# Kernel optimization log

Measured on AMD Instinct MI355X. Metric: run time of the kernel, lower is better.

Reference implementation:

```python
import jax, jax.numpy as jnp
import numpy as np

DIM = 1024
NUM_HEADS = 16
HEAD_DIM = DIM // NUM_HEADS


def _rope(x):
    # x: (B*H, L, hd). ESM-style rotary embedding with rotate_half.
    L, hd = x.shape[1], x.shape[2]
    inv_freq = 1.0 / (10000.0 ** (jnp.arange(0, hd, 2, dtype=jnp.float32) / hd))
    t = jnp.arange(L, dtype=jnp.float32)
    freqs = t[:, None] * inv_freq[None, :]          # (L, hd/2)
    emb = jnp.concatenate([freqs, freqs], axis=-1)   # (L, hd)
    cos, sin = jnp.cos(emb), jnp.sin(emb)
    x1, x2 = jnp.split(x, 2, axis=-1)
    rot = jnp.concatenate([-x2, x1], axis=-1)
    return x * cos + rot * sin


def setup_inputs() -> dict:
    key = jax.random.key(0)
    ks = jax.random.split(key, 10)
    L, N, D = 2048, 1, DIM
    query = jax.random.normal(ks[0], (L, N, D), dtype=jnp.float32)
    asym_ids = jnp.sort(jax.random.randint(ks[1], (N, L), 0, 4), axis=-1)
    s = 0.02
    wq = s * jax.random.normal(ks[2], (D, D), dtype=jnp.float32)
    wk = s * jax.random.normal(ks[3], (D, D), dtype=jnp.float32)
    wv = s * jax.random.normal(ks[4], (D, D), dtype=jnp.float32)
    wo = s * jax.random.normal(ks[5], (D, D), dtype=jnp.float32)
    bq = s * jax.random.normal(ks[6], (D,), dtype=jnp.float32)
    bk = s * jax.random.normal(ks[7], (D,), dtype=jnp.float32)
    bv = s * jax.random.normal(ks[8], (D,), dtype=jnp.float32)
    bo = s * jax.random.normal(ks[9], (D,), dtype=jnp.float32)
    return {"query": query, "asym_ids": asym_ids, "wq": wq, "bq": bq,
            "wk": wk, "bk": bk, "wv": wv, "bv": bv, "wo": wo, "bo": bo}


def reference(query, asym_ids, wq, bq, wk, bk, wv, bv, wo, bo):
    L, N, D = query.shape
    H, hd = NUM_HEADS, HEAD_DIM
    scaling = 1.0 / np.sqrt(hd)

    q = (query @ wq.T + bq) * scaling
    k = query @ wk.T + bk
    v = query @ wv.T + bv

    def to_bh(x):  # (L, N, D) -> (N*H, L, hd)
        return x.reshape(L, N * H, hd).transpose(1, 0, 2)

    q, k, v = to_bh(q), to_bh(k), to_bh(v)

    # raw scores (pre-RoPE), rpe scores (post-RoPE)
    raw = jnp.einsum('ble,bme->blm', q, k).reshape(N, H, L, L)
    qr, kr = _rope(q), _rope(k)
    rpe = jnp.einsum('ble,bme->blm', qr, kr).reshape(N, H, L, L)

    avg = jnp.mean(rpe - raw, axis=(0, 1), keepdims=True)          # (1,1,L,L)
    asym_mask = asym_ids[:, :, None] == asym_ids[:, None, :]        # (N,L,L)
    attn_weights = jnp.where(asym_mask[:, None], rpe, raw + avg)    # (N,H,L,L)

    probs = jax.nn.softmax(attn_weights, axis=-1)
    attn = jnp.einsum('nhlm,nhme->nhle', probs, v.reshape(N, H, L, hd))
    attn = attn.transpose(2, 0, 1, 3).reshape(L, N, D)
    out = attn @ wo.T + bo
    attn_weights_avg = jnp.mean(probs, axis=1)  # (N, L, L)
    return out, attn_weights_avg
```

## Files before the change

### kernel.cpp

```cpp
#include <hip/hip_runtime.h>
#include <hip/hip_bf16.h>

#define L 2048
#define D 1024
#define NH 16
#define HD 64
#define SPLIT 4
#define JCH (L / SPLIT)
#define LOG2E 1.4426950408889634f

typedef __attribute__((ext_vector_type(8))) short bf16x8;
typedef __attribute__((ext_vector_type(4))) float f32x4;

#define MFMA(a, b, c) __builtin_amdgcn_mfma_f32_16x16x32_bf16(a, b, c, 0, 0, 0)

__device__ __forceinline__ short f2bf(float x) {
  __hip_bfloat16 h = __float2bfloat16(x);
  return *reinterpret_cast<short*>(&h);
}

__device__ __forceinline__ void gll16(const void* g, void* l) {
  __builtin_amdgcn_global_load_lds(
      (const __attribute__((address_space(1))) void*)(uintptr_t)g,
      (__attribute__((address_space(3))) void*)(unsigned)(uintptr_t)l, 16, 0, 0);
}

__global__ void prep_kernel(const float* __restrict__ q,
                            const float* __restrict__ w0, const float* __restrict__ w1,
                            const float* __restrict__ w2, const float* __restrict__ w3,
                            float* __restrict__ costab, float* __restrict__ sintab,
                            short* __restrict__ dq, short* __restrict__ d0,
                            short* __restrict__ d1, short* __restrict__ d2,
                            short* __restrict__ d3) {
  int i = blockIdx.x * 256 + threadIdx.x;
  if (i < 65536) {
    int t = i >> 5, fi = i & 31;
    float f = exp2f(-(float)fi * (13.287712379549449f / 32.0f));
    float ang = (float)t * f;
    costab[i] = cosf(ang);
    sintab[i] = sinf(ang);
    return;
  }
  int i2 = i - 65536;
  const float* src;
  short* dst;
  int off;
  if (i2 < L * D / 4) {
    src = q; dst = dq; off = i2;
  } else {
    int j = i2 - L * D / 4;
    int seg = j >> 18;
    off = j & (262144 - 1);
    src = seg == 0 ? w0 : seg == 1 ? w1 : seg == 2 ? w2 : w3;
    dst = seg == 0 ? d0 : seg == 1 ? d1 : seg == 2 ? d2 : d3;
  }
  float4 v = ((const float4*)src)[off];
  short4 o;
  o.x = f2bf(v.x); o.y = f2bf(v.y); o.z = f2bf(v.z); o.w = f2bf(v.w);
  ((short4*)dst)[off] = o;
}

__global__ __launch_bounds__(256) void proj3_kernel(
    const short* __restrict__ X,
    const short* __restrict__ Wq, const short* __restrict__ Wk, const short* __restrict__ Wv,
    const float* __restrict__ bq, const float* __restrict__ bk, const float* __restrict__ bv,
    const float* __restrict__ costab, const float* __restrict__ sintab,
    short* __restrict__ Qs, short* __restrict__ QRb, short* __restrict__ Kbb,
    short* __restrict__ KRb, short* __restrict__ Vt) {
  int mode = blockIdx.z;
  const short* W = mode == 0 ? Wq : (mode == 1 ? Wk : Wv);
  const float* bias = mode == 0 ? bq : (mode == 1 ? bk : bv);
  short* out_main = mode == 0 ? Qs : (mode == 1 ? Kbb : Vt);
  short* out_rope = mode == 0 ? QRb : KRb;

  int w = threadIdx.x >> 6, lane = threadIdx.x & 63;
  int c = lane & 15, g = lane >> 4;
  int wi0 = blockIdx.y * 128 + w * 32;
  int wj0 = blockIdx.x * 64;

  f32x4 acc[2][4];
#pragma unroll
  for (int m = 0; m < 2; ++m)
#pragma unroll
    for (int n = 0; n < 4; ++n) acc[m][n] = (f32x4){0.f, 0.f, 0.f, 0.f};

  for (int k0 = 0; k0 < D; k0 += 32) {
    bf16x8 aF[2], bF[4];
#pragma unroll
    for (int m = 0; m < 2; ++m)
      aF[m] = *(const bf16x8*)(X + (size_t)(wi0 + m * 16 + c) * D + k0 + g * 8);
#pragma unroll
    for (int n = 0; n < 4; ++n)
      bF[n] = *(const bf16x8*)(W + (size_t)(wj0 + n * 16 + c) * D + k0 + g * 8);
#pragma unroll
    for (int m = 0; m < 2; ++m)
#pragma unroll
      for (int n = 0; n < 4; ++n) acc[m][n] = MFMA(aF[m], bF[n], acc[m][n]);
  }

  float scale = (mode == 0) ? 0.125f * LOG2E : 1.0f;
#pragma unroll
  for (int m = 0; m < 2; ++m) {
#pragma unroll
    for (int r = 0; r < 4; ++r) {
      int i = wi0 + m * 16 + g * 4 + r;
      float v4[4];
#pragma unroll
      for (int n = 0; n < 4; ++n)
        v4[n] = (acc[m][n][r] + bias[wj0 + n * 16 + c]) * scale;
      if (mode == 2) {
#pragma unroll
        for (int n = 0; n < 4; ++n) {
          int col = wj0 + n * 16 + c;
          out_main[(size_t)col * L + i] = f2bf(v4[n]);
        }
      } else {
#pragma unroll
        for (int n = 0; n < 4; ++n) {
          int col = wj0 + n * 16 + c;
          out_main[(size_t)i * D + col] = f2bf(v4[n]);
          float rot = (n < 2) ? -v4[n + 2] : v4[n - 2];
          int fidx = i * 32 + (n & 1) * 16 + c;
          float vr = v4[n] * costab[fidx] + rot * sintab[fidx];
          out_rope[(size_t)i * D + col] = f2bf(vr);
        }
      }
    }
  }
}

__global__ __launch_bounds__(256) void avg_kernel(
    const short* __restrict__ QR, const short* __restrict__ KR,
    const short* __restrict__ Qs, const short* __restrict__ Kb,
    const int* __restrict__ ids, f32x4* __restrict__ avg4) {
  int ib = blockIdx.y * 128, jb = blockIdx.x * 64;
  if (ids[ib] == ids[ib + 127] && ids[jb] == ids[jb + 63] && ids[ib] == ids[jb])
    return;

  int w = threadIdx.x >> 6, lane = threadIdx.x & 63;
  int c = lane & 15, g = lane >> 4;
  int wi0 = ib + (w >> 1) * 64;
  int wj0 = jb + (w & 1) * 32;

  f32x4 acc1[4][2], acc2[4][2];
#pragma unroll
  for (int m = 0; m < 4; ++m)
#pragma unroll
    for (int n = 0; n < 2; ++n) {
      acc1[m][n] = (f32x4){0.f, 0.f, 0.f, 0.f};
      acc2[m][n] = (f32x4){0.f, 0.f, 0.f, 0.f};
    }

  for (int k0 = 0; k0 < D; k0 += 32) {
    bf16x8 aF[4], a2F[4], bF[2], b2F[2];
#pragma unroll
    for (int m = 0; m < 4; ++m) {
      aF[m] = *(const bf16x8*)(QR + (size_t)(wi0 + m * 16 + c) * D + k0 + g * 8);
      a2F[m] = *(const bf16x8*)(Qs + (size_t)(wi0 + m * 16 + c) * D + k0 + g * 8);
    }
#pragma unroll
    for (int n = 0; n < 2; ++n) {
      bF[n] = *(const bf16x8*)(KR + (size_t)(wj0 + n * 16 + c) * D + k0 + g * 8);
      b2F[n] = *(const bf16x8*)(Kb + (size_t)(wj0 + n * 16 + c) * D + k0 + g * 8);
    }
#pragma unroll
    for (int m = 0; m < 4; ++m)
#pragma unroll
      for (int n = 0; n < 2; ++n) {
        acc1[m][n] = MFMA(aF[m], bF[n], acc1[m][n]);
        acc2[m][n] = MFMA(a2F[m], b2F[n], acc2[m][n]);
      }
  }

#pragma unroll
  for (int m = 0; m < 4; ++m)
#pragma unroll
    for (int n = 0; n < 2; ++n) {
      int j = wj0 + n * 16 + c;
      f32x4 o;
#pragma unroll
      for (int r = 0; r < 4; ++r) o[r] = (acc1[m][n][r] - acc2[m][n][r]) * 0.0625f;
      avg4[(size_t)(((wi0 + m * 16) >> 2) + g) * L + j] = o;
    }
}

__global__ __launch_bounds__(256) void flash3_kernel(
    const short* __restrict__ Qs, const short* __restrict__ Kb,
    const short* __restrict__ QR, const short* __restrict__ KR,
    const short* __restrict__ Vt, const f32x4* __restrict__ avg4,
    const int* __restrict__ ids, float* __restrict__ m_part,
    float* __restrict__ l_part, float* __restrict__ acc_part) {
  int dd = blockIdx.x + 32 * (blockIdx.y + NH * blockIdx.z);
  int xcd = dd & 7, slot = dd >> 3;
  int xblk = xcd * 4 + (slot & 3);
  int hs = slot >> 2;
  int h = hs & (NH - 1), sp = hs >> 4;

  int w = threadIdx.x >> 6, lane = threadIdx.x & 63;
  int c = lane & 15, g = lane >> 4;
  int i0 = xblk * 64 + w * 16;
  int hk = h * 64;

  __shared__ short kb_lds[2][64 * 64];
  __shared__ short kr_lds[2][64 * 64];
  __shared__ short plds[4][16][64];

  int srow = lane >> 3;
  int sxor = (lane & 7) ^ srow;
  int r0a = w * 16, r0b = w * 16 + 8;

  bf16x8 qA[2], qrA[2];
  {
    const short* qp = Qs + (size_t)(i0 + c) * D + hk + g * 8;
    const short* qrp = QR + (size_t)(i0 + c) * D + hk + g * 8;
    qA[0] = *(const bf16x8*)qp;   qA[1] = *(const bf16x8*)(qp + 32);
    qrA[0] = *(const bf16x8*)qrp; qrA[1] = *(const bf16x8*)(qrp + 32);
  }

  int idi[4];
  float mrun[4], lsum[4];
  f32x4 acc[4];
#pragma unroll
  for (int r = 0; r < 4; ++r) {
    idi[r] = ids[i0 + g * 4 + r];
    mrun[r] = -3.0e38f;
    lsum[r] = 0.f;
  }
#pragma unroll
  for (int n = 0; n < 4; ++n) acc[n] = (f32x4){0.f, 0.f, 0.f, 0.f};

  int ifirst = __shfl(idi[0], 0);
  bool iu = __all((idi[0] == idi[1]) & (idi[1] == idi[2]) & (idi[2] == idi[3]) &
                  (idi[0] == ifirst));

  const f32x4* avrow = avg4 + (size_t)((i0 >> 2) + g) * L;
  int jbase = sp * JCH;
  const int NT = JCH / 64;

  gll16(Kb + (size_t)(jbase + r0a + srow) * D + hk + sxor * 8, &kb_lds[0][r0a * 64]);
  gll16(Kb + (size_t)(jbase + r0b + srow) * D + hk + sxor * 8, &kb_lds[0][r0b * 64]);
  gll16(KR + (size_t)(jbase + r0a + srow) * D + hk + sxor * 8, &kr_lds[0][r0a * 64]);
  gll16(KR + (size_t)(jbase + r0b + srow) * D + hk + sxor * 8, &kr_lds[0][r0b * 64]);

  f32x4 avn[4];
  int idjn[4];
#pragma unroll
  for (int sub = 0; sub < 4; ++sub) {
    avn[sub] = avrow[jbase + sub * 16 + c];
    idjn[sub] = ids[jbase + sub * 16 + c];
  }
  __syncthreads();

  int cur = 0;
  for (int jt = 0; jt < NT; ++jt) {
    int jb = jbase + jt * 64;

    if (jt + 1 < NT) {
      int jn = jb + 64;
      short* kd = &kb_lds[cur ^ 1][0];
      short* rd = &kr_lds[cur ^ 1][0];
      gll16(Kb + (size_t)(jn + r0a + srow) * D + hk + sxor * 8, kd + r0a * 64);
      gll16(Kb + (size_t)(jn + r0b + srow) * D + hk + sxor * 8, kd + r0b * 64);
      gll16(KR + (size_t)(jn + r0a + srow) * D + hk + sxor * 8, rd + r0a * 64);
      gll16(KR + (size_t)(jn + r0b + srow) * D + hk + sxor * 8, rd + r0b * 64);
    }

    bf16x8 vf0[4], vf1[4];
#pragma unroll
    for (int n = 0; n < 4; ++n) {
      const short* vp = Vt + (size_t)(hk + n * 16 + c) * L + jb + g * 8;
      vf0[n] = *(const bf16x8*)vp;
      vf1[n] = *(const bf16x8*)(vp + 32);
    }

    f32x4 av[4];
    int idj[4];
#pragma unroll
    for (int sub = 0; sub < 4; ++sub) { av[sub] = avn[sub]; idj[sub] = idjn[sub]; }
    if (jt + 1 < NT) {
#pragma unroll
      for (int sub = 0; sub < 4; ++sub) {
        avn[sub] = avrow[jb + 64 + sub * 16 + c];
        idjn[sub] = ids[jb + 64 + sub * 16 + c];
      }
    }

    int jfirst = __shfl(idj[0], 0);
    bool ju = __all((idj[0] == idj[1]) & (idj[1] == idj[2]) & (idj[2] == idj[3]) &
                    (idj[0] == jfirst));

    const short* kbb = &kb_lds[cur][c * 64];
    const short* krb = &kr_lds[cur][c * 64];
    int co0 = (g ^ (c & 7)) * 8;
    int co1 = ((4 + g) ^ (c & 7)) * 8;

    float t[4][4];
    if (iu && ju && ifirst == jfirst) {
#pragma unroll
      for (int sub = 0; sub < 4; ++sub) {
        bf16x8 kr0 = *(const bf16x8*)(krb + sub * 1024 + co0);
        bf16x8 kr1 = *(const bf16x8*)(krb + sub * 1024 + co1);
        f32x4 z = (f32x4){0.f, 0.f, 0.f, 0.f};
        f32x4 rp = MFMA(qrA[1], kr1, MFMA(qrA[0], kr0, z));
#pragma unroll
        for (int r = 0; r < 4; ++r) t[sub][r] = rp[r];
      }
    } else if (iu && ju) {
#pragma unroll
      for (int sub = 0; sub < 4; ++sub) {
        bf16x8 k0 = *(const bf16x8*)(kbb + sub * 1024 + co0);
        bf16x8 k1 = *(const bf16x8*)(kbb + sub * 1024 + co1);
        f32x4 z = (f32x4){0.f, 0.f, 0.f, 0.f};
        f32x4 rw = MFMA(qA[1], k1, MFMA(qA[0], k0, z));
#pragma unroll
        for (int r = 0; r < 4; ++r) t[sub][r] = rw[r] + av[sub][r];
      }
    } else {
#pragma unroll
      for (int sub = 0; sub < 4; ++sub) {
        bf16x8 k0 = *(const bf16x8*)(kbb + sub * 1024 + co0);
        bf16x8 k1 = *(const bf16x8*)(kbb + sub * 1024 + co1);
        bf16x8 kr0 = *(const bf16x8*)(krb + sub * 1024 + co0);
        bf16x8 kr1 = *(const bf16x8*)(krb + sub * 1024 + co1);
        f32x4 z = (f32x4){0.f, 0.f, 0.f, 0.f};
        f32x4 rw = MFMA(qA[1], k1, MFMA(qA[0], k0, z));
        f32x4 rp = MFMA(qrA[1], kr1, MFMA(qrA[0], kr0, z));
#pragma unroll
        for (int r = 0; r < 4; ++r)
          t[sub][r] = (idi[r] == idj[sub]) ? rp[r] : (rw[r] + av[sub][r]);
      }
    }

    float tm[4];
#pragma unroll
    for (int r = 0; r < 4; ++r)
      tm[r] = fmaxf(fmaxf(t[0][r], t[1][r]), fmaxf(t[2][r], t[3][r]));
    bool ok = (tm[0] <= mrun[0] + 8.f) && (tm[1] <= mrun[1] + 8.f) &&
              (tm[2] <= mrun[2] + 8.f) && (tm[3] <= mrun[3] + 8.f);
    if (!__all(ok)) {
#pragma unroll
      for (int r = 0; r < 4; ++r) {
        float m2 = tm[r];
#pragma unroll
        for (int d = 1; d < 16; d <<= 1) m2 = fmaxf(m2, __shfl_xor(m2, d));
        float mn = fmaxf(mrun[r], m2);
        float so = exp2f(mrun[r] - mn);
        mrun[r] = mn;
        lsum[r] *= so;
#pragma unroll
        for (int n = 0; n < 4; ++n) acc[n][r] *= so;
      }
    }

#pragma unroll
    for (int sub = 0; sub < 4; ++sub)
#pragma unroll
      for (int r = 0; r < 4; ++r) {
        float p = exp2f(t[sub][r] - mrun[r]);
        lsum[r] += p;
        int prow = g * 4 + r;
        plds[w][prow][(sub * 16 + c) ^ ((prow & 7) << 3)] = f2bf(p);
      }

    {
      int pc0 = (g * 8) ^ ((c & 7) << 3);
      int pc1 = (32 + g * 8) ^ ((c & 7) << 3);
      bf16x8 pa = *(const bf16x8*)(&plds[w][c][pc0]);
#pragma unroll
      for (int n = 0; n < 4; ++n) acc[n] = MFMA(pa, vf0[n], acc[n]);
      bf16x8 pb = *(const bf16x8*)(&plds[w][c][pc1]);
#pragma unroll
      for (int n = 0; n < 4; ++n) acc[n] = MFMA(pb, vf1[n], acc[n]);
    }

    __syncthreads();
    cur ^= 1;
  }

#pragma unroll
  for (int r = 0; r < 4; ++r) {
#pragma unroll
    for (int d = 1; d < 16; d <<= 1) lsum[r] += __shfl_xor(lsum[r], d);
  }
  size_t sb = (size_t)(sp * NH + h) * L;
  if (c == 0) {
#pragma unroll
    for (int r = 0; r < 4; ++r) {
      m_part[sb + i0 + g * 4 + r] = mrun[r];
      l_part[sb + i0 + g * 4 + r] = lsum[r];
    }
  }
#pragma unroll
  for (int n = 0; n < 4; ++n)
#pragma unroll
    for (int r = 0; r < 4; ++r)
      acc_part[(sb + i0 + g * 4 + r) * HD + n * 16 + c] = acc[n][r];
}

__global__ void merge_kernel(const float* __restrict__ m_part,
                             const float* __restrict__ l_part,
                             const float* __restrict__ acc_part,
                             float* __restrict__ mfin, float* __restrict__ lfin,
                             short* __restrict__ attn_bf) {
  int idx = blockIdx.x * 256 + threadIdx.x;
  int d = idx & (HD - 1);
  int hi = idx >> 6;
  int i = hi & (L - 1), h = hi >> 11;
  float m4 = -3.0e38f;
#pragma unroll
  for (int s = 0; s < SPLIT; ++s)
    m4 = fmaxf(m4, m_part[(size_t)(s * NH + h) * L + i]);
  float l = 0.f, o = 0.f;
#pragma unroll
  for (int s = 0; s < SPLIT; ++s) {
    size_t sb = (size_t)(s * NH + h) * L + i;
    float e = exp2f(m_part[sb] - m4);
    l += l_part[sb] * e;
    o += acc_part[sb * HD + d] * e;
  }
  attn_bf[(size_t)i * D + h * HD + d] = f2bf(o / l);
  if (d == 0) { mfin[h * L + i] = m4; lfin[h * L + i] = l; }
}

__global__ __launch_bounds__(256) void pavgout_kernel(
    const short* __restrict__ Qs, const short* __restrict__ Kb,
    const short* __restrict__ QR, const short* __restrict__ KR,
    const f32x4* __restrict__ avg4, const int* __restrict__ ids,
    const float* __restrict__ m_ws, const float* __restrict__ l_ws,
    float* __restrict__ out1,
    const short* __restrict__ A, const short* __restrict__ W,
    const float* __restrict__ bias, float* __restrict__ out0) {
  __shared__ short kb_lds[2][64 * 64];
  __shared__ short kr_lds[2][64 * 64];
  __shared__ float mS[NH][64], lS[NH][64];

  int bid = blockIdx.x;
  int w = threadIdx.x >> 6, lane = threadIdx.x & 63;
  int c = lane & 15, g = lane >> 4;

  if (bid >= 1024) {
    int idx = bid - 1024;
    int wj0 = (idx & 15) * 64 + (w & 1) * 32;
    int wi0 = (idx >> 4) * 64 + (w >> 1) * 32;

    f32x4 acc[2][2];
#pragma unroll
    for (int m = 0; m < 2; ++m)
#pragma unroll
      for (int n = 0; n < 2; ++n) acc[m][n] = (f32x4){0.f, 0.f, 0.f, 0.f};

    for (int k0 = 0; k0 < D; k0 += 32) {
      bf16x8 aF[2], bF[2];
#pragma unroll
      for (int m = 0; m < 2; ++m)
        aF[m] = *(const bf16x8*)(A + (size_t)(wi0 + m * 16 + c) * D + k0 + g * 8);
#pragma unroll
      for (int n = 0; n < 2; ++n)
        bF[n] = *(const bf16x8*)(W + (size_t)(wj0 + n * 16 + c) * D + k0 + g * 8);
#pragma unroll
      for (int m = 0; m < 2; ++m)
#pragma unroll
        for (int n = 0; n < 2; ++n) acc[m][n] = MFMA(aF[m], bF[n], acc[m][n]);
    }

#pragma unroll
    for (int m = 0; m < 2; ++m)
#pragma unroll
      for (int n = 0; n < 2; ++n)
#pragma unroll
        for (int r = 0; r < 4; ++r) {
          int i = wi0 + m * 16 + g * 4 + r;
          int col = wj0 + n * 16 + c;
          out0[(size_t)i * D + col] = acc[m][n][r] + bias[col];
        }
    return;
  }

  int xcd = bid & 7, slot = bid >> 3;
  int iidx = xcd * 4 + (slot & 3);
  int jidx = slot >> 2;
  int j0 = jidx * 64;
  int iblk = iidx * 64;
  int i0 = iblk + w * 16;

  int srow = lane >> 3;
  int sxor = (lane & 7) ^ srow;
  int r0a = w * 16, r0b = w * 16 + 8;

  int si0 = ids[iblk], si1 = ids[iblk + 63];
  int sj0 = ids[j0], sj1 = ids[j0 + 63];
  int mode = (si0 == si1 && sj0 == sj1) ? ((si0 == sj0) ? 0 : 1) : 2;

  for (int idx = threadIdx.x; idx < NH * 64; idx += 256) {
    int hh = idx >> 6, rr = idx & 63;
    mS[hh][rr] = m_ws[hh * L + iblk + rr];
    lS[hh][rr] = 1.0f / l_ws[hh * L + iblk + rr];
  }

  if (mode != 0) {
    gll16(Kb + (size_t)(j0 + r0a + srow) * D + sxor * 8, &kb_lds[0][r0a * 64]);
    gll16(Kb + (size_t)(j0 + r0b + srow) * D + sxor * 8, &kb_lds[0][r0b * 64]);
  }
  if (mode != 1) {
    gll16(KR + (size_t)(j0 + r0a + srow) * D + sxor * 8, &kr_lds[0][r0a * 64]);
    gll16(KR + (size_t)(j0 + r0b + srow) * D + sxor * 8, &kr_lds[0][r0b * 64]);
  }

  int idi[4], idj[4];
  f32x4 av[4];
  {
    const f32x4* avrow = avg4 + (size_t)((i0 >> 2) + g) * L;
#pragma unroll
    for (int sub = 0; sub < 4; ++sub) {
      av[sub] = avrow[j0 + sub * 16 + c];
      idj[sub] = ids[j0 + sub * 16 + c];
    }
#pragma unroll
    for (int r = 0; r < 4; ++r) idi[r] = ids[i0 + g * 4 + r];
  }

  f32x4 psum[4];
#pragma unroll
  for (int sub = 0; sub < 4; ++sub) psum[sub] = (f32x4){0.f, 0.f, 0.f, 0.f};

  const short* qbase = Qs + (size_t)(i0 + c) * D + g * 8;
  const short* qrbase = QR + (size_t)(i0 + c) * D + g * 8;

  bf16x8 nq0, nq1, nqr0, nqr1;
  if (mode != 0) { nq0 = *(const bf16x8*)qbase; nq1 = *(const bf16x8*)(qbase + 32); }
  if (mode != 1) { nqr0 = *(const bf16x8*)qrbase; nqr1 = *(const bf16x8*)(qrbase + 32); }

  __syncthreads();

  int cur = 0;
#pragma unroll 1
  for (int hh = 0; hh < NH; ++hh) {
    if (hh + 1 < NH) {
      int hkn = (hh + 1) * 64;
      short* kd = &kb_lds[cur ^ 1][0];
      short* rd = &kr_lds[cur ^ 1][0];
      if (mode != 0) {
        gll16(Kb + (size_t)(j0 + r0a + srow) * D + hkn + sxor * 8, kd + r0a * 64);
        gll16(Kb + (size_t)(j0 + r0b + srow) * D + hkn + sxor * 8, kd + r0b * 64);
      }
      if (mode != 1) {
        gll16(KR + (size_t)(j0 + r0a + srow) * D + hkn + sxor * 8, rd + r0a * 64);
        gll16(KR + (size_t)(j0 + r0b + srow) * D + hkn + sxor * 8, rd + r0b * 64);
      }
    }

    bf16x8 q0 = nq0, q1 = nq1, qr0 = nqr0, qr1 = nqr1;
    if (hh + 1 < NH) {
      int hkn = (hh + 1) * 64;
      if (mode != 0) {
        nq0 = *(const bf16x8*)(qbase + hkn);
        nq1 = *(const bf16x8*)(qbase + hkn + 32);
      }
      if (mode != 1) {
        nqr0 = *(const bf16x8*)(qrbase + hkn);
        nqr1 = *(const bf16x8*)(qrbase + hkn + 32);
      }
    }

    const short* kbb = &kb_lds[cur][c * 64];
    const short* krb = &kr_lds[cur][c * 64];
    int co0 = (g ^ (c & 7)) * 8;
    int co1 = ((4 + g) ^ (c & 7)) * 8;

    f32x4 m4 = *(const f32x4*)(&mS[hh][w * 16 + g * 4]);
    f32x4 l4 = *(const f32x4*)(&lS[hh][w * 16 + g * 4]);

    if (mode == 0) {
#pragma unroll
      for (int sub = 0; sub < 4; ++sub) {
        bf16x8 kr0 = *(const bf16x8*)(krb + sub * 1024 + co0);
        bf16x8 kr1 = *(const bf16x8*)(krb + sub * 1024 + co1);
        f32x4 z = (f32x4){0.f, 0.f, 0.f, 0.f};
        f32x4 rp = MFMA(qr1, kr1, MFMA(qr0, kr0, z));
#pragma unroll
        for (int r = 0; r < 4; ++r)
          psum[sub][r] += exp2f(rp[r] - m4[r]) * l4[r];
      }
    } else if (mode == 1) {
#pragma unroll
      for (int sub = 0; sub < 4; ++sub) {
        bf16x8 k0 = *(const bf16x8*)(kbb + sub * 1024 + co0);
        bf16x8 k1 = *(const bf16x8*)(kbb + sub * 1024 + co1);
        f32x4 z = (f32x4){0.f, 0.f, 0.f, 0.f};
        f32x4 rw = MFMA(q1, k1, MFMA(q0, k0, z));
#pragma unroll
        for (int r = 0; r < 4; ++r)
          psum[sub][r] += exp2f(rw[r] + av[sub][r] - m4[r]) * l4[r];
      }
    } else {
#pragma unroll
      for (int sub = 0; sub < 4; ++sub) {
        bf16x8 k0 = *(const bf16x8*)(kbb + sub * 1024 + co0);
        bf16x8 k1 = *(const bf16x8*)(kbb + sub * 1024 + co1);
        bf16x8 kr0 = *(const bf16x8*)(krb + sub * 1024 + co0);
        bf16x8 kr1 = *(const bf16x8*)(krb + sub * 1024 + co1);
        f32x4 z = (f32x4){0.f, 0.f, 0.f, 0.f};
        f32x4 rw = MFMA(q1, k1, MFMA(q0, k0, z));
        f32x4 rp = MFMA(qr1, kr1, MFMA(qr0, kr0, z));
#pragma unroll
        for (int r = 0; r < 4; ++r) {
          float s = (idi[r] == idj[sub]) ? rp[r] : (rw[r] + av[sub][r]);
          psum[sub][r] += exp2f(s - m4[r]) * l4[r];
        }
      }
    }

    __syncthreads();
    cur ^= 1;
  }

#pragma unroll
  for (int sub = 0; sub < 4; ++sub)
#pragma unroll
    for (int r = 0; r < 4; ++r)
      out1[(size_t)(i0 + g * 4 + r) * L + j0 + sub * 16 + c] = psum[sub][r] * 0.0625f;
}

extern "C" void kernel_launch(void* const* d_in, const int* in_sizes, int n_in,
                              void* d_out, int out_size, void* d_ws, size_t ws_size,
                              hipStream_t stream) {
  const float* query = (const float*)d_in[0];
  const int* ids = (const int*)d_in[1];
  const float* wq = (const float*)d_in[2];
  const float* bq = (const float*)d_in[3];
  const float* wk = (const float*)d_in[4];
  const float* bk = (const float*)d_in[5];
  const float* wv = (const float*)d_in[6];
  const float* bv = (const float*)d_in[7];
  const float* wo = (const float*)d_in[8];
  const float* bo = (const float*)d_in[9];

  char* p = (char*)d_ws;
  auto carve = [&](size_t bytes) {
    char* r = p;
    p += (bytes + 255) & ~(size_t)255;
    return r;
  };
  short* Xbf = (short*)carve((size_t)L * D * 2);
  short* Wqb = (short*)carve((size_t)D * D * 2);
  short* Wkb = (short*)carve((size_t)D * D * 2);
  short* Wvb = (short*)carve((size_t)D * D * 2);
  short* Wob = (short*)carve((size_t)D * D * 2);
  short* Qs = (short*)carve((size_t)L * D * 2);
  short* QRb = (short*)carve((size_t)L * D * 2);
  short* Kbb = (short*)carve((size_t)L * D * 2);
  short* KRb = (short*)carve((size_t)L * D * 2);
  short* Vt = (short*)carve((size_t)L * D * 2);
  f32x4* avg4 = (f32x4*)carve((size_t)L * L * 4);
  float* m_ws = (float*)carve((size_t)NH * L * 4);
  float* l_ws = (float*)carve((size_t)NH * L * 4);
  short* attn_bf = (short*)carve((size_t)L * D * 2);
  float* costab = (float*)carve((size_t)L * 32 * 4);
  float* sintab = (float*)carve((size_t)L * 32 * 4);
  float* m_part = (float*)carve((size_t)SPLIT * NH * L * 4);
  float* l_part = (float*)carve((size_t)SPLIT * NH * L * 4);
  float* acc_part = (float*)carve((size_t)SPLIT * NH * L * HD * 4);

  float* out0 = (float*)d_out;
  float* out1 = out0 + (size_t)L * D;

  prep_kernel<<<(65536 + L * D / 4 + 4 * (D * D / 4)) / 256, 256, 0, stream>>>(
      query, wq, wk, wv, wo, costab, sintab, Xbf, Wqb, Wkb, Wvb, Wob);

  proj3_kernel<<<dim3(D / 64, L / 128, 3), 256, 0, stream>>>(
      Xbf, Wqb, Wkb, Wvb, bq, bk, bv, costab, sintab, Qs, QRb, Kbb, KRb, Vt);

  avg_kernel<<<dim3(L / 64, L / 128), 256, 0, stream>>>(QRb, KRb, Qs, Kbb, ids, avg4);

  flash3_kernel<<<dim3(L / 64, NH, SPLIT), 256, 0, stream>>>(
      Qs, Kbb, QRb, KRb, Vt, avg4, ids, m_part, l_part, acc_part);

  merge_kernel<<<(NH * L * HD) / 256, 256, 0, stream>>>(m_part, l_part, acc_part,
                                                        m_ws, l_ws, attn_bf);

  pavgout_kernel<<<1536, 256, 0, stream>>>(Qs, Kbb, QRb, KRb, avg4, ids,
                                           m_ws, l_ws, out1, attn_bf, Wob, bo, out0);
}
```

Baseline: 344.9 us.

## Store fp16 attention scores in flash pass and reuse them for probability averaging

The flash kernel now writes every masked score to a new fp16 workspace buffer of shape 16×L×L. A new tail kernel turns those stored scores into averaged probabilities with the final max and sum, and fuses in the output projection. This removes the second recomputation of QK and RoPE scores that pavgout did. In exchange it adds about 128 MB of global writes plus the same amount of reads, the scores are rounded to fp16, and the path only runs if the workspace is large enough.

```diff
diff --git a/kernel.cpp b/kernel.cpp
--- a/kernel.cpp
+++ b/kernel.cpp
@@ -17,6 +17,19 @@
 __device__ __forceinline__ short f2bf(float x) {
   __hip_bfloat16 h = __float2bfloat16(x);
   return *reinterpret_cast<short*>(&h);
+}
+
+__device__ __forceinline__ short f2h(float x) {
+  _Float16 hv = (_Float16)x;
+  short s;
+  __builtin_memcpy(&s, &hv, 2);
+  return s;
+}
+
+__device__ __forceinline__ float h2f(short s) {
+  _Float16 hv;
+  __builtin_memcpy(&hv, &s, 2);
+  return (float)hv;
 }
 
 __device__ __forceinline__ void gll16(const void* g, void* l) {
@@ -189,7 +202,8 @@
     const short* __restrict__ QR, const short* __restrict__ KR,
     const short* __restrict__ Vt, const f32x4* __restrict__ avg4,
     const int* __restrict__ ids, float* __restrict__ m_part,
-    float* __restrict__ l_part, float* __restrict__ acc_part) {
+    float* __restrict__ l_part, float* __restrict__ acc_part,
+    short* __restrict__ Sbuf) {
   int dd = blockIdx.x + 32 * (blockIdx.y + NH * blockIdx.z);
   int xcd = dd & 7, slot = dd >> 3;
   int xblk = xcd * 4 + (slot & 3);
@@ -232,6 +246,8 @@
   int ifirst = __shfl(idi[0], 0);
   bool iu = __all((idi[0] == idi[1]) & (idi[1] == idi[2]) & (idi[2] == idi[3]) &
                   (idi[0] == ifirst));
+
+  size_t srow_base = ((size_t)h * L + (size_t)(i0 + g * 4)) * L + c;
 
   const f32x4* avrow = avg4 + (size_t)((i0 >> 2) + g) * L;
   int jbase = sp * JCH;
@@ -329,6 +345,14 @@
         for (int r = 0; r < 4; ++r)
           t[sub][r] = (idi[r] == idj[sub]) ? rp[r] : (rw[r] + av[sub][r]);
       }
+    }
+
+    if (Sbuf) {
+#pragma unroll
+      for (int sub = 0; sub < 4; ++sub)
+#pragma unroll
+        for (int r = 0; r < 4; ++r)
+          Sbuf[srow_base + (size_t)r * L + jb + sub * 16] = f2h(t[sub][r]);
     }
 
     float tm[4];
@@ -420,6 +444,74 @@
   }
   attn_bf[(size_t)i * D + h * HD + d] = f2bf(o / l);
   if (d == 0) { mfin[h * L + i] = m4; lfin[h * L + i] = l; }
+}
+
+__global__ __launch_bounds__(256) void tail2_kernel(
+    const short* __restrict__ S, const float* __restrict__ m_ws,
+    const float* __restrict__ l_ws, float* __restrict__ out1,
+    const short* __restrict__ A, const short* __restrict__ W,
+    const float* __restrict__ bias, float* __restrict__ out0) {
+  int bid = blockIdx.x;
+  int w = threadIdx.x >> 6, lane = threadIdx.x & 63;
+  int c = lane & 15, g = lane >> 4;
+
+  if (bid >= L) {
+    int idx = bid - L;
+    int wj0 = (idx & 15) * 64 + (w & 1) * 32;
+    int wi0 = (idx >> 4) * 64 + (w >> 1) * 32;
+
+    f32x4 acc[2][2];
+#pragma unroll
+    for (int m = 0; m < 2; ++m)
+#pragma unroll
+      for (int n = 0; n < 2; ++n) acc[m][n] = (f32x4){0.f, 0.f, 0.f, 0.f};
+
+    for (int k0 = 0; k0 < D; k0 += 32) {
+      bf16x8 aF[2], bF[2];
+#pragma unroll
+      for (int m = 0; m < 2; ++m)
+        aF[m] = *(const bf16x8*)(A + (size_t)(wi0 + m * 16 + c) * D + k0 + g * 8);
+#pragma unroll
+      for (int n = 0; n < 2; ++n)
+        bF[n] = *(const bf16x8*)(W + (size_t)(wj0 + n * 16 + c) * D + k0 + g * 8);
+#pragma unroll
+      for (int m = 0; m < 2; ++m)
+#pragma unroll
+        for (int n = 0; n < 2; ++n) acc[m][n] = MFMA(aF[m], bF[n], acc[m][n]);
+    }
+
+#pragma unroll
+    for (int m = 0; m < 2; ++m)
+#pragma unroll
+      for (int n = 0; n < 2; ++n)
+#pragma unroll
+        for (int r = 0; r < 4; ++r) {
+          int i = wi0 + m * 16 + g * 4 + r;
+          int col = wj0 + n * 16 + c;
+          out0[(size_t)i * D + col] = acc[m][n][r] + bias[col];
+        }
+    return;
+  }
+
+  int i = bid;
+  int j0 = threadIdx.x * 8;
+  float ps[8] = {0.f, 0.f, 0.f, 0.f, 0.f, 0.f, 0.f, 0.f};
+
+#pragma unroll 1
+  for (int h = 0; h < NH; ++h) {
+    float m = m_ws[h * L + i];
+    float linv = 1.0f / l_ws[h * L + i];
+    bf16x8 sv = *(const bf16x8*)(S + ((size_t)h * L + i) * L + j0);
+#pragma unroll
+    for (int k = 0; k < 8; ++k)
+      ps[k] += exp2f(h2f((short)sv[k]) - m) * linv;
+  }
+
+  float4 o0 = {ps[0] * 0.0625f, ps[1] * 0.0625f, ps[2] * 0.0625f, ps[3] * 0.0625f};
+  float4 o1 = {ps[4] * 0.0625f, ps[5] * 0.0625f, ps[6] * 0.0625f, ps[7] * 0.0625f};
+  float* dst = out1 + (size_t)i * L + j0;
+  *(float4*)dst = o0;
+  *(float4*)(dst + 4) = o1;
 }
 
 __global__ __launch_bounds__(256) void pavgout_kernel(
@@ -661,6 +753,11 @@
   float* l_part = (float*)carve((size_t)SPLIT * NH * L * 4);
   float* acc_part = (float*)carve((size_t)SPLIT * NH * L * HD * 4);
 
+  size_t used = (size_t)(p - (char*)d_ws);
+  size_t s_bytes = (size_t)NH * L * L * 2;
+  short* Sbuf = nullptr;
+  if (ws_size >= used + s_bytes + 4096) Sbuf = (short*)carve(s_bytes);
+
   float* out0 = (float*)d_out;
   float* out1 = out0 + (size_t)L * D;
 
@@ -673,11 +770,16 @@
   avg_kernel<<<dim3(L / 64, L / 128), 256, 0, stream>>>(QRb, KRb, Qs, Kbb, ids, avg4);
 
   flash3_kernel<<<dim3(L / 64, NH, SPLIT), 256, 0, stream>>>(
-      Qs, Kbb, QRb, KRb, Vt, avg4, ids, m_part, l_part, acc_part);
+      Qs, Kbb, QRb, KRb, Vt, avg4, ids, m_part, l_part, acc_part, Sbuf);
 
   merge_kernel<<<(NH * L * HD) / 256, 256, 0, stream>>>(m_part, l_part, acc_part,
                                                         m_ws, l_ws, attn_bf);
 
-  pavgout_kernel<<<1536, 256, 0, stream>>>(Qs, Kbb, QRb, KRb, avg4, ids,
-                                           m_ws, l_ws, out1, attn_bf, Wob, bo, out0);
-}
+  if (Sbuf) {
+    tail2_kernel<<<L + 512, 256, 0, stream>>>(Sbuf, m_ws, l_ws, out1,
+                                              attn_bf, Wob, bo, out0);
+  } else {
+    pavgout_kernel<<<1536, 256, 0, stream>>>(Qs, Kbb, QRb, KRb, avg4, ids,
+                                             m_ws, l_ws, out1, attn_bf, Wob, bo, out0);
+  }
+}
```

After: 350.3 us. About the same (+1.6%).
